# Optimization experiments

Measured on AMD Instinct MI355X. Metric: run time of the kernel, lower is better.

Reference implementation:

```python
import jax, jax.numpy as jnp
import numpy as np

B, D, H, W = 8, 64, 128, 128
N = B * H * W            # 131072 flat pixels
P = N // 16              # 8192 positives (fixed positive ratio)
TEMP = 0.07
EPS = 1e-12


def _l2norm(x):
    # F.normalize(x, p=2, dim=1): x / max(||x||, eps)
    n = jnp.sqrt(jnp.sum(x * x, axis=1, keepdims=True))
    return x / jnp.maximum(n, EPS)


def setup_inputs() -> dict:
    key = jax.random.key(0)
    rng = np.random.default_rng(0)
    perm = rng.permutation(N)
    pos_global = np.sort(perm[:P]).astype(np.int32)          # flat indices of mask==1
    neg_global = np.sort(perm[P:]).astype(np.int32)          # flat indices of mask==0
    num_neg = neg_global.shape[0]                            # 122880

    # mask consistent with the index sets (order b,h,w matches mask.view(-1))
    mask_flat = np.zeros(N, np.float32)
    mask_flat[pos_global] = 1.0
    mask = mask_flat.reshape(B, 1, H, W)

    # negative_sampling_ratio = 0.5
    S = max(1, int(num_neg * 0.5))                           # 61440
    neg_idx = neg_global[rng.permutation(num_neg)[:S]]
    # anchors: int(P * 0.5) local indices into positives
    A = min(P, int(P * 0.5))                                 # 4096
    anchor_idx = rng.permutation(P)[:A].astype(np.int32)
    # accuracy stat samples (sample_ratio = 0.1, min 10)
    nap = max(10, int(P * 0.1))                              # 819
    nan = max(10, int(num_neg * 0.1))                        # 12288
    acc_pos_idx = pos_global[rng.permutation(P)[:nap]]
    acc_neg_idx = neg_global[rng.permutation(num_neg)[:nan]]

    z = jax.random.normal(key, (B, D, H, W), dtype=jnp.float32)
    return {
        "z": z,
        "mask": jnp.asarray(mask),
        "pos_idx": jnp.asarray(pos_global),
        "anchor_idx": jnp.asarray(anchor_idx),
        "neg_idx": jnp.asarray(neg_idx),
        "acc_pos_idx": jnp.asarray(acc_pos_idx),
        "acc_neg_idx": jnp.asarray(acc_neg_idx),
    }


def reference(z, mask, pos_idx, anchor_idx, neg_idx, acc_pos_idx, acc_neg_idx):
    b, d, h, w = z.shape
    z_flat = z.transpose(0, 2, 3, 1).reshape(-1, d)          # (N, D)

    # ---- MaskGuidedContrastiveLoss (vectorized) ----
    pos = _l2norm(z_flat[pos_idx])                           # (P, D)
    neg = _l2norm(z_flat[neg_idx])                           # (S, D)
    anchors = pos[anchor_idx]                                # (A, D)

    sim_pos = jnp.einsum('ad,pd->ap', anchors, pos) / TEMP   # (A, P)
    sim_neg = jnp.einsum('ad,sd->as', anchors, neg) / TEMP   # (A, S)

    A = anchors.shape[0]
    ar = jnp.arange(A)
    # torch loop excludes column i for anchor i (i < P always here)
    sim_pos_noself = sim_pos.at[ar, ar].set(-jnp.inf)
    pos_sim = jnp.max(sim_pos_noself, axis=1)                # (A,)
    lse = jax.nn.logsumexp(
        jnp.concatenate([pos_sim[:, None], sim_neg], axis=1), axis=1)
    loss = jnp.mean(lse - pos_sim)

    # ---- stats (no_grad in torch) ----
    ap = _l2norm(z_flat[acc_pos_idx])                        # (np_, D)
    an = _l2norm(z_flat[acc_neg_idx])                        # (nn_, D)
    np_ = ap.shape[0]
    spp = jnp.einsum('id,jd->ij', ap, ap)
    spp = spp.at[jnp.arange(np_), jnp.arange(np_)].set(0.0)
    per_pos = jnp.sum(spp, axis=1) / (np_ - 1)
    per_neg = jnp.mean(jnp.einsum('id,jd->ij', ap, an), axis=1)
    accuracy = jnp.mean((per_pos > per_neg).astype(jnp.float32))
    positive_ratio = jnp.mean((mask > 0.5).astype(jnp.float32))

    return loss, accuracy, positive_ratio
```

## Files before the change

### kernel.cpp

```cpp
#include <hip/hip_runtime.h>
#include <math.h>

#define HW_SHIFT 14
#define HW_MASK 16383
#define TEMP_INV 14.285714285714285714f
#define M0F TEMP_INV
#define CEXP_S 20.609929155556627f
#define CEXP_B (-20.609929155556627f)

#define NCP 32
#define NCN 64
#define NB_AP 16
#define NB_AN 64
#define AF 4

typedef __attribute__((ext_vector_type(8))) short short8v;
typedef __attribute__((ext_vector_type(4))) float f32x4;

__device__ inline ushort f2bf(float f) {
    uint u = __float_as_uint(f);
    return (ushort)((u + 0x7FFFu + ((u >> 16) & 1u)) >> 16);
}
__device__ inline float bf2f(ushort b) { return __uint_as_float((uint)b << 16); }

#define GLOAD_LDS16(g, l) __builtin_amdgcn_global_load_lds( \
    (const __attribute__((address_space(1))) void*)(g), \
    (__attribute__((address_space(3))) void*)(l), 16, 0, 0)

__global__ void k_norm_cat(const float* __restrict__ z, const int* __restrict__ idx,
                           int count, ushort* __restrict__ outCat) {
    int lane = threadIdx.x & 63;
    int wstride = (blockDim.x >> 6) * gridDim.x;
    for (int w = blockIdx.x * (blockDim.x >> 6) + (threadIdx.x >> 6); w < count; w += wstride) {
        int n = idx[w];
        int b = n >> HW_SHIFT;
        int hw = n & HW_MASK;
        float v = z[((size_t)(b * 64 + lane) << HW_SHIFT) + hw];
        float ss = v * v;
#pragma unroll
        for (int o = 32; o >= 1; o >>= 1) ss += __shfl_xor(ss, o, 64);
        float x = v / fmaxf(sqrtf(ss), 1e-12f);
        ushort hi = f2bf(x);
        outCat[(size_t)w * 128 + lane] = hi;
        outCat[(size_t)w * 128 + 64 + lane] = f2bf(x - bf2f(hi));
    }
}

__global__ void k_norm_f32(const float* __restrict__ z, const int* __restrict__ idx,
                           int count, float* __restrict__ out) {
    int lane = threadIdx.x & 63;
    int wstride = (blockDim.x >> 6) * gridDim.x;
    for (int w = blockIdx.x * (blockDim.x >> 6) + (threadIdx.x >> 6); w < count; w += wstride) {
        int n = idx[w];
        int b = n >> HW_SHIFT;
        int hw = n & HW_MASK;
        float v = z[((size_t)(b * 64 + lane) << HW_SHIFT) + hw];
        float ss = v * v;
#pragma unroll
        for (int o = 32; o >= 1; o >>= 1) ss += __shfl_xor(ss, o, 64);
        out[((size_t)w << 6) + lane] = v / fmaxf(sqrtf(ss), 1e-12f);
    }
}

template <int MODE>
__global__ void __launch_bounds__(256) k_sim_mfma(
    const ushort* __restrict__ posCat, const int* __restrict__ aidx, int A,
    const ushort* __restrict__ cand, int count, int per,
    float* __restrict__ partial) {
    __shared__ __align__(16) char ldsB[8192];

    int wid = threadIdx.x >> 6;
    int lane = threadIdx.x & 63;
    int lrow = lane & 15;
    int q = lane >> 4;
    int a0 = blockIdx.x * 256 + wid * 64;
    int chunk = blockIdx.y;
    int c0 = chunk * per;
    int c1 = min(count, c0 + per);
    int nsteps = (c1 > c0) ? ((c1 - c0 + 31) >> 5) : 0;

    short8v af[AF][4];
#pragma unroll
    for (int g = 0; g < AF; ++g) {
        int arow = a0 + g * 16 + lrow;
        int asrc = aidx[min(arow, A - 1)];
        const ushort* aptr = posCat + (size_t)asrc * 128 + q * 8;
#pragma unroll
        for (int s = 0; s < 4; ++s) af[g][s] = *(const short8v*)(aptr + 32 * s);
    }

    float rs[AF][4];
#pragma unroll
    for (int g = 0; g < AF; ++g)
#pragma unroll
        for (int e = 0; e < 4; ++e) rs[g][e] = (MODE == 0) ? -3.0e38f : 0.f;

    auto stage = [&](int t) {
        const char* gsrc = (const char*)cand + (size_t)(c0 + t * 32) * 256;
#pragma unroll
        for (int i = 0; i < 2; ++i) {
            uint ubase = (uint)i * 4096u + (uint)wid * 1024u;
            uint o = ubase + (uint)lane * 16u;
            uint row = o >> 8;
            uint src = o ^ ((row & 7u) << 4);
            GLOAD_LDS16(gsrc + src, ldsB + ubase);
        }
    };

    auto computeTile = [&](int t16, int tglob) {
        short8v b[4];
#pragma unroll
        for (int s = 0; s < 4; ++s) {
            uint row = (uint)(t16 * 16 + lrow);
            uint col = (uint)(q * 16 + s * 64);
            uint addr = row * 256u + (col ^ ((row & 7u) << 4));
            b[s] = *(const short8v*)(ldsB + addr);
        }
        int colg = c0 + tglob * 16 + lrow;
        bool colok = colg < c1;
#pragma unroll
        for (int g = 0; g < AF; ++g) {
            f32x4 acc = {0.f, 0.f, 0.f, 0.f};
            acc = __builtin_amdgcn_mfma_f32_16x16x32_bf16(af[g][0], b[0], acc, 0, 0, 0);
            acc = __builtin_amdgcn_mfma_f32_16x16x32_bf16(af[g][1], b[1], acc, 0, 0, 0);
            acc = __builtin_amdgcn_mfma_f32_16x16x32_bf16(af[g][0], b[2], acc, 0, 0, 0);
            acc = __builtin_amdgcn_mfma_f32_16x16x32_bf16(af[g][1], b[3], acc, 0, 0, 0);
            acc = __builtin_amdgcn_mfma_f32_16x16x32_bf16(af[g][2], b[0], acc, 0, 0, 0);
            acc = __builtin_amdgcn_mfma_f32_16x16x32_bf16(af[g][3], b[1], acc, 0, 0, 0);
#pragma unroll
            for (int e = 0; e < 4; ++e) {
                if (MODE == 0) {
                    int rowg = a0 + g * 16 + q * 4 + e;
                    float l = acc[e] * TEMP_INV;
                    if (!colok || rowg == colg) l = -3.0e38f;
                    rs[g][e] = fmaxf(rs[g][e], l);
                } else {
                    float p = exp2f(__fmaf_rn(acc[e], CEXP_S, CEXP_B));
                    rs[g][e] += colok ? p : 0.f;
                }
            }
        }
    };

    for (int t = 0; t < nsteps; ++t) {
        stage(t);
        __syncthreads();
        computeTile(0, 2 * t);
        computeTile(1, 2 * t + 1);
        __syncthreads();
    }

#pragma unroll
    for (int g = 0; g < AF; ++g) {
#pragma unroll
        for (int e = 0; e < 4; ++e) {
            float v = rs[g][e];
#pragma unroll
            for (int o = 8; o >= 1; o >>= 1) {
                float w = __shfl_xor(v, o, 64);
                v = (MODE == 0) ? fmaxf(v, w) : (v + w);
            }
            rs[g][e] = v;
        }
        if (lrow == 0) {
            int rbase = a0 + g * 16 + q * 4;
#pragma unroll
            for (int e = 0; e < 4; ++e)
                if (rbase + e < A) partial[(size_t)chunk * A + rbase + e] = rs[g][e];
        }
    }
}

__global__ void k_combine(const float* __restrict__ posmax, int ncp,
                          const float* __restrict__ negsum, int ncn,
                          int A, float* __restrict__ lossPartial) {
    int a = blockIdx.x * blockDim.x + threadIdx.x;
    float term = 0.f;
    if (a < A) {
        float m = -__builtin_inff();
        for (int k = 0; k < ncp; ++k) m = fmaxf(m, posmax[(size_t)k * A + a]);
        float s = 0.f;
        for (int k = 0; k < ncn; ++k) s += negsum[(size_t)k * A + a];
        term = M0F + logf(__expf(m - M0F) + s) - m;
    }
    __shared__ float red[256];
    red[threadIdx.x] = term;
    __syncthreads();
    for (int o = 128; o >= 1; o >>= 1) {
        if (threadIdx.x < o) red[threadIdx.x] += red[threadIdx.x + o];
        __syncthreads();
    }
    if (threadIdx.x == 0) lossPartial[blockIdx.x] = red[0];
}

__global__ void k_colsum(const float* __restrict__ in, int rows, float* __restrict__ partial) {
    int d = threadIdx.x & 63;
    int rg = threadIdx.x >> 6;
    float acc = 0.f;
    for (int r = blockIdx.x * 4 + rg; r < rows; r += gridDim.x * 4)
        acc += in[((size_t)r << 6) + d];
    __shared__ float red[256];
    red[threadIdx.x] = acc;
    __syncthreads();
    if (rg == 0)
        partial[((size_t)blockIdx.x << 6) + d] = (red[d] + red[64 + d]) + (red[128 + d] + red[192 + d]);
}

__global__ void k_colsum_final(const float* __restrict__ partial, int nb, float* __restrict__ out64) {
    int d = threadIdx.x;
    if (d >= 64) return;
    float acc = 0.f;
    for (int k = 0; k < nb; ++k) acc += partial[((size_t)k << 6) + d];
    out64[d] = acc;
}

__global__ void k_acc(const float* __restrict__ ap, int nap, int nan_,
                      const float* __restrict__ Sp, const float* __restrict__ Sn,
                      int* __restrict__ accCount) {
    int i = blockIdx.x * (blockDim.x >> 6) + (threadIdx.x >> 6);
    int d = threadIdx.x & 63;
    if (i >= nap) return;
    float v = ap[((size_t)i << 6) + d];
    float dsp = v * Sp[d];
    float dse = v * v;
    float dsn = v * Sn[d];
#pragma unroll
    for (int o = 32; o >= 1; o >>= 1) {
        dsp += __shfl_xor(dsp, o, 64);
        dse += __shfl_xor(dse, o, 64);
        dsn += __shfl_xor(dsn, o, 64);
    }
    if (d == 0) {
        float per_pos = (dsp - dse) / (float)(nap - 1);
        float per_neg = dsn / (float)nan_;
        if (per_pos > per_neg) atomicAdd(accCount, 1);
    }
}

__global__ void k_mask(const float* __restrict__ mask, int n, int* __restrict__ cnt) {
    int t = blockIdx.x * blockDim.x + threadIdx.x;
    int local = 0;
    for (int i = t; i < n; i += gridDim.x * blockDim.x) local += (mask[i] > 0.5f) ? 1 : 0;
#pragma unroll
    for (int o = 32; o >= 1; o >>= 1) local += __shfl_xor(local, o, 64);
    __shared__ int red[4];
    if ((threadIdx.x & 63) == 0) red[threadIdx.x >> 6] = local;
    __syncthreads();
    if (threadIdx.x == 0) atomicAdd(cnt, red[0] + red[1] + red[2] + red[3]);
}

__global__ void k_init(int* p) {
    if (threadIdx.x < 2) p[threadIdx.x] = 0;
}

__global__ void k_out(const float* __restrict__ lossPartial, int nb, int A,
                      const int* __restrict__ accCount, int nap,
                      const int* __restrict__ maskCount, int n,
                      float* __restrict__ out) {
    if (threadIdx.x != 0 || blockIdx.x != 0) return;
    float ls = 0.f;
    for (int k = 0; k < nb; ++k) ls += lossPartial[k];
    out[0] = ls / (float)A;
    out[1] = (float)(*accCount) / (float)nap;
    out[2] = (float)(*maskCount) / (float)n;
}

extern "C" void kernel_launch(void* const* d_in, const int* in_sizes, int n_in,
                              void* d_out, int out_size, void* d_ws, size_t ws_size,
                              hipStream_t stream) {
    const float* z        = (const float*)d_in[0];
    const float* mask     = (const float*)d_in[1];
    const int* pos_idx    = (const int*)d_in[2];
    const int* anchor_idx = (const int*)d_in[3];
    const int* neg_idx    = (const int*)d_in[4];
    const int* acc_pos_idx= (const int*)d_in[5];
    const int* acc_neg_idx= (const int*)d_in[6];
    float* out = (float*)d_out;

    const int N   = in_sizes[1];
    const int P   = in_sizes[2];
    const int A   = in_sizes[3];
    const int S   = in_sizes[4];
    const int NAP = in_sizes[5];
    const int NAN_= in_sizes[6];

    float* ws = (float*)d_ws;
    size_t off = 0;
    auto alloc = [&](size_t floats) { size_t p = off; off += (floats + 63) & ~(size_t)63; return p; };

    size_t o_posCat = alloc((size_t)(P + 32) * 64);
    size_t o_negCat = alloc((size_t)(S + 32) * 64);
    size_t o_apN    = alloc((size_t)NAP * 64);
    size_t o_anN    = alloc((size_t)NAN_ * 64);
    size_t o_posmax = alloc((size_t)NCP * A);
    size_t o_negsum = alloc((size_t)NCN * A);
    size_t o_lossP  = alloc(64);
    size_t o_spPart = alloc((size_t)NB_AP * 64);
    size_t o_snPart = alloc((size_t)NB_AN * 64);
    size_t o_Sp     = alloc(64);
    size_t o_Sn     = alloc(64);
    size_t o_cnt    = alloc(64);

    ushort* posCat = (ushort*)(ws + o_posCat);
    ushort* negCat = (ushort*)(ws + o_negCat);
    float* apN = ws + o_apN;
    float* anN = ws + o_anN;
    float* posmax = ws + o_posmax;
    float* negsum = ws + o_negsum;
    float* lossPartial = ws + o_lossP;
    float* spPart = ws + o_spPart;
    float* snPart = ws + o_snPart;
    float* Sp = ws + o_Sp;
    float* Sn = ws + o_Sn;
    int* counters = (int*)(ws + o_cnt);

    k_init<<<1, 64, 0, stream>>>(counters);

    k_norm_cat<<<dim3(1024), 256, 0, stream>>>(z, pos_idx, P, posCat);
    k_norm_cat<<<dim3(2048), 256, 0, stream>>>(z, neg_idx, S, negCat);
    k_norm_f32<<<dim3(256), 256, 0, stream>>>(z, acc_pos_idx, NAP, apN);
    k_norm_f32<<<dim3(512), 256, 0, stream>>>(z, acc_neg_idx, NAN_, anN);

    int gx = (A + 255) / 256;
    int perP = (P + NCP - 1) / NCP;
    int perN = (S + NCN - 1) / NCN;
    k_sim_mfma<0><<<dim3(gx, NCP), 256, 0, stream>>>(posCat, anchor_idx, A, posCat, P, perP, posmax);
    k_sim_mfma<1><<<dim3(gx, NCN), 256, 0, stream>>>(posCat, anchor_idx, A, negCat, S, perN, negsum);

    int nLossBlk = (A + 255) / 256;
    k_combine<<<dim3(nLossBlk), 256, 0, stream>>>(posmax, NCP, negsum, NCN, A, lossPartial);

    k_colsum<<<dim3(NB_AP), 256, 0, stream>>>(apN, NAP, spPart);
    k_colsum_final<<<1, 64, 0, stream>>>(spPart, NB_AP, Sp);
    k_colsum<<<dim3(NB_AN), 256, 0, stream>>>(anN, NAN_, snPart);
    k_colsum_final<<<1, 64, 0, stream>>>(snPart, NB_AN, Sn);
    k_acc<<<dim3((NAP + 3) / 4), 256, 0, stream>>>(apN, NAP, NAN_, Sp, Sn, counters);

    k_mask<<<dim3(256), 256, 0, stream>>>(mask, N, counters + 1);

    k_out<<<1, 64, 0, stream>>>(lossPartial, nLossBlk, A, counters, NAP, counters + 1, N, out);
}
```

Measured before the change: 307.7 us.

## Simplify LDS staging layout, hoist address math, double chunk counts, skip interior masking

Drops the XOR swizzle and precomputes per-lane global and LDS offsets, so each lane reads its B fragment straight from a transposed LDS layout with constant strides. Interior tiles in the negative-sum mode skip the column bounds check. The positive-max mode now defers the temperature scaling to the final store. The positive and negative chunk counts are doubled for more parallelism, at the cost of more partials for the combine step and a possible rise in LDS bank conflicts without the swizzle.

Result: slower. 341.6 us (+11.0%).

```diff
diff --git a/kernel.cpp b/kernel.cpp
--- a/kernel.cpp
+++ b/kernel.cpp
@@ -8,8 +8,8 @@
 #define CEXP_S 20.609929155556627f
 #define CEXP_B (-20.609929155556627f)
 
-#define NCP 32
-#define NCN 64
+#define NCP 64
+#define NCN 128
 #define NB_AP 16
 #define NB_AN 64
 #define AF 4
@@ -95,29 +95,21 @@
 #pragma unroll
         for (int e = 0; e < 4; ++e) rs[g][e] = (MODE == 0) ? -3.0e38f : 0.f;
 
+    uint gofs = (uint)lrow * 256u + (uint)q * 16u + (uint)wid * 64u;
+    uint ub = (uint)wid * 1024u;
+    uint vaddr = (uint)q * 256u + (uint)lrow * 16u;
+
     auto stage = [&](int t) {
         const char* gsrc = (const char*)cand + (size_t)(c0 + t * 32) * 256;
-#pragma unroll
-        for (int i = 0; i < 2; ++i) {
-            uint ubase = (uint)i * 4096u + (uint)wid * 1024u;
-            uint o = ubase + (uint)lane * 16u;
-            uint row = o >> 8;
-            uint src = o ^ ((row & 7u) << 4);
-            GLOAD_LDS16(gsrc + src, ldsB + ubase);
-        }
+        GLOAD_LDS16(gsrc + gofs, ldsB + ub);
+        GLOAD_LDS16(gsrc + gofs + 4096u, ldsB + ub + 4096u);
     };
 
     auto computeTile = [&](int t16, int tglob) {
         short8v b[4];
-#pragma unroll
-        for (int s = 0; s < 4; ++s) {
-            uint row = (uint)(t16 * 16 + lrow);
-            uint col = (uint)(q * 16 + s * 64);
-            uint addr = row * 256u + (col ^ ((row & 7u) << 4));
-            b[s] = *(const short8v*)(ldsB + addr);
-        }
-        int colg = c0 + tglob * 16 + lrow;
-        bool colok = colg < c1;
+        const char* lb = ldsB + vaddr + (uint)t16 * 4096u;
+#pragma unroll
+        for (int s = 0; s < 4; ++s) b[s] = *(const short8v*)(lb + s * 1024);
 #pragma unroll
         for (int g = 0; g < AF; ++g) {
             f32x4 acc = {0.f, 0.f, 0.f, 0.f};
@@ -127,16 +119,29 @@
             acc = __builtin_amdgcn_mfma_f32_16x16x32_bf16(af[g][1], b[3], acc, 0, 0, 0);
             acc = __builtin_amdgcn_mfma_f32_16x16x32_bf16(af[g][2], b[0], acc, 0, 0, 0);
             acc = __builtin_amdgcn_mfma_f32_16x16x32_bf16(af[g][3], b[1], acc, 0, 0, 0);
-#pragma unroll
-            for (int e = 0; e < 4; ++e) {
-                if (MODE == 0) {
+            if (MODE == 1) {
+                bool interior = (c0 + tglob * 16 + 16) <= c1;
+                if (interior) {
+#pragma unroll
+                    for (int e = 0; e < 4; ++e)
+                        rs[g][e] += exp2f(__fmaf_rn(acc[e], CEXP_S, CEXP_B));
+                } else {
+                    int colg = c0 + tglob * 16 + lrow;
+                    bool colok = colg < c1;
+#pragma unroll
+                    for (int e = 0; e < 4; ++e) {
+                        float p = exp2f(__fmaf_rn(acc[e], CEXP_S, CEXP_B));
+                        rs[g][e] += colok ? p : 0.f;
+                    }
+                }
+            } else {
+                int colg = c0 + tglob * 16 + lrow;
+                bool colok = colg < c1;
+#pragma unroll
+                for (int e = 0; e < 4; ++e) {
                     int rowg = a0 + g * 16 + q * 4 + e;
-                    float l = acc[e] * TEMP_INV;
-                    if (!colok || rowg == colg) l = -3.0e38f;
-                    rs[g][e] = fmaxf(rs[g][e], l);
-                } else {
-                    float p = exp2f(__fmaf_rn(acc[e], CEXP_S, CEXP_B));
-                    rs[g][e] += colok ? p : 0.f;
+                    float v = (!colok || rowg == colg) ? -3.0e38f : acc[e];
+                    rs[g][e] = fmaxf(rs[g][e], v);
                 }
             }
         }
@@ -166,7 +171,11 @@
             int rbase = a0 + g * 16 + q * 4;
 #pragma unroll
             for (int e = 0; e < 4; ++e)
-                if (rbase + e < A) partial[(size_t)chunk * A + rbase + e] = rs[g][e];
+                if (rbase + e < A) {
+                    float v = rs[g][e];
+                    if (MODE == 0) v *= TEMP_INV;
+                    partial[(size_t)chunk * A + rbase + e] = v;
+                }
         }
     }
 }
```
